# Kernel optimization log

Hardware: AMD Instinct MI355X
Metric: run time of the kernel (lower is better)

Reference implementation:

```python
import jax, jax.numpy as jnp
import numpy as np

MARGIN = 0.3
PD_EPS = 1e-6  # torch F.pairwise_distance adds eps to the difference


def setup_inputs() -> dict:
    key = jax.random.key(0)
    k1, k2 = jax.random.split(key)
    B, D, NUM_CLASSES = 8192, 256, 8
    embeddings = jax.random.normal(k1, (B, D), dtype=jnp.float32)
    labels = jax.random.randint(k2, (B,), 0, NUM_CLASSES, dtype=jnp.int64)
    return {"embeddings": embeddings, "labels": labels}


def _pairwise_euclidean(x):
    # cdist(x, x, p=2) via the Gram trick; clamp tiny negatives before sqrt
    sq = jnp.sum(x * x, axis=1)  # [B]
    d2 = sq[:, None] + sq[None, :] - 2.0 * (x @ x.T)
    return jnp.sqrt(jnp.maximum(d2, 0.0))


def reference(embeddings, labels):
    B = embeddings.shape[0]
    D = _pairwise_euclidean(embeddings)  # [B, B]

    eq = labels[:, None] == labels[None, :]
    eye = jnp.eye(B, dtype=bool)
    pos_mask = eq & ~eye          # same label, not self
    neg_mask = ~eq                # different label

    # hard mining: per anchor, farthest positive and closest negative
    pos_idx = jnp.argmax(jnp.where(pos_mask, D, -jnp.inf), axis=1)  # [B]
    neg_idx = jnp.argmin(jnp.where(neg_mask, D, jnp.inf), axis=1)   # [B]
    valid = pos_mask.any(axis=1) & neg_mask.any(axis=1)             # [B]

    # recompute triplet distances like F.pairwise_distance (eps on the diff)
    pos_dist = jnp.linalg.norm(embeddings - embeddings[pos_idx] + PD_EPS, axis=1)
    neg_dist = jnp.linalg.norm(embeddings - embeddings[neg_idx] + PD_EPS, axis=1)

    per_anchor = jax.nn.relu(pos_dist - neg_dist + MARGIN)
    n_valid = jnp.maximum(valid.sum(), 1)
    loss = jnp.sum(jnp.where(valid, per_anchor, 0.0)) / n_valid.astype(per_anchor.dtype)
    return loss
```

## Files before the change

kernel.cpp:

```cpp
#include <hip/hip_runtime.h>
#include <math.h>


typedef __attribute__((ext_vector_type(8))) short short8;
typedef __attribute__((ext_vector_type(4))) float floatx4;

#define B_N 8192
#define D_K 256

__device__ __forceinline__ unsigned short f2bf_rne(float f) {
  unsigned u = __float_as_uint(f);
  u += 0x7FFFu + ((u >> 16) & 1u);
  return (unsigned short)(u >> 16);
}

__global__ void k_split(const float* __restrict__ x, unsigned short* __restrict__ xhf,
                        float* __restrict__ sqq,
                        float* __restrict__ sum, int* __restrict__ cnt,
                        int* __restrict__ done) {
  __shared__ float sw[64];
  const int tid  = threadIdx.x;
  const int lane = tid & 63;
  const int w    = tid >> 6;
  const int b    = blockIdx.x;
  const int m    = lane & 15;
  const int quad = lane >> 4;
  const int row  = b * 16 + m;

  float s = 0.f;
#pragma unroll
  for (int h = 0; h < 2; ++h) {
    int tk = w + h * 4;
    int kk = tk * 32 + quad * 8;
    float4 f0 = *reinterpret_cast<const float4*>(x + (size_t)row * D_K + kk);
    float4 f1 = *reinterpret_cast<const float4*>(x + (size_t)row * D_K + kk + 4);
    s += f0.x * f0.x + f0.y * f0.y + f0.z * f0.z + f0.w * f0.w;
    s += f1.x * f1.x + f1.y * f1.y + f1.z * f1.z + f1.w * f1.w;
    ushort4 lo, hi;
    lo.x = f2bf_rne(f0.x); lo.y = f2bf_rne(f0.y); lo.z = f2bf_rne(f0.z); lo.w = f2bf_rne(f0.w);
    hi.x = f2bf_rne(f1.x); hi.y = f2bf_rne(f1.y); hi.z = f2bf_rne(f1.z); hi.w = f2bf_rne(f1.w);
    size_t o = ((size_t)b * 8 + tk) * 512 + lane * 8;
    *reinterpret_cast<ushort4*>(xhf + o)     = lo;
    *reinterpret_cast<ushort4*>(xhf + o + 4) = hi;
  }
  s += __shfl_xor(s, 16);
  s += __shfl_xor(s, 32);
  if (quad == 0) sw[w * 16 + m] = s;
  __syncthreads();
  if (tid < 16) {
    int i = b * 16 + tid;
    float t = sw[tid] + sw[16 + tid] + sw[32 + tid] + sw[48 + tid];
    sqq[i] = fmaf(t, 128.f, 262144.f);
  }
  if (b == 0 && tid == 0) { *sum = 0.f; *cnt = 0; *done = 0; }
}

__global__ __launch_bounds__(256) void k_mine15(
    const unsigned short* __restrict__ xhf, const int* __restrict__ lab,
    const float* __restrict__ sqq,
    unsigned* __restrict__ ppart, unsigned* __restrict__ npart) {
  __shared__ unsigned short Alds[8 * 8 * 512];

  int t  = blockIdx.x;
  int bi = (int)(64.5f - sqrtf(64.5f * 64.5f - 2.f * (float)t));
  int b0 = 64 * bi - (bi * (bi - 1)) / 2;
  if (t < b0) { bi--; b0 = 64 * bi - (bi * (bi - 1)) / 2; }
  else {
    int b1 = 64 * (bi + 1) - ((bi + 1) * bi) / 2;
    if (t >= b1) { bi++; b0 = b1; }
  }
  const int bj = bi + (t - b0);

  const int tid  = threadIdx.x;
  const int lane = tid & 63;
  const int w    = tid >> 6;
  const int wi   = w >> 1, wj = w & 1;
  const int quad = lane >> 4, l15 = lane & 15;
  const int i0   = bi * 128;

  {
    const short8* src = reinterpret_cast<const short8*>(xhf + (size_t)bi * 32768);
    short8* dst = reinterpret_cast<short8*>(Alds);
#pragma unroll
    for (int it = 0; it < 16; ++it) dst[it * 256 + tid] = src[it * 256 + tid];
  }

  unsigned pkey[16], nkey[16];
  unsigned lip0 = 0, lip1 = 0;
  float    sqi[16];
#pragma unroll
  for (int r = 0; r < 16; ++r) {
    pkey[r] = 0u; nkey[r] = 0xFFFFFFFFu;
    int ir = i0 + wi * 64 + (r >> 2) * 16 + quad * 4 + (r & 3);
    unsigned lv = (unsigned)lab[ir] & 0xFu;
    if (r < 8) lip0 |= lv << (r * 4); else lip1 |= lv << ((r - 8) * 4);
    sqi[r] = sqq[ir];
  }
  __syncthreads();

  const unsigned short* Bw = xhf + ((size_t)(bj * 8 + wj * 4) * 8) * 512 + lane * 8;
  const unsigned short* Aw = Alds + (size_t)wi * 32 * 512 + lane * 8;

  floatx4 acc[16];
#pragma unroll
  for (int q = 0; q < 16; ++q) acc[q] = (floatx4)0.f;

#pragma unroll
  for (int tk = 0; tk < 8; ++tk) {
    short8 Bf[4];
#pragma unroll
    for (int nt = 0; nt < 4; ++nt)
      Bf[nt] = *reinterpret_cast<const short8*>(Bw + nt * 4096 + tk * 512);
    short8 Af[4];
#pragma unroll
    for (int mt = 0; mt < 4; ++mt)
      Af[mt] = *reinterpret_cast<const short8*>(Aw + (size_t)(mt * 8 + tk) * 512);
#pragma unroll
    for (int mt = 0; mt < 4; ++mt)
#pragma unroll
      for (int nt = 0; nt < 4; ++nt)
        acc[mt * 4 + nt] = __builtin_amdgcn_mfma_f32_16x16x32_bf16(
            Af[mt], Bf[nt], acc[mt * 4 + nt], 0, 0, 0);
  }

#pragma unroll
  for (int nt = 0; nt < 4; ++nt) {
    int      j  = bj * 128 + wj * 64 + nt * 16 + l15;
    unsigned jl = (unsigned)lab[j] & 0xFu;
    float    sj = sqq[j];
    unsigned jp = 0u, jn = 0xFFFFFFFFu;
#pragma unroll
    for (int r = 0; r < 16; ++r) {
      int mt = r >> 2, reg = r & 3;
      float dot = acc[mt * 4 + nt][reg];
      int   ir  = i0 + wi * 64 + mt * 16 + quad * 4 + reg;
      unsigned lr = (r < 8 ? (lip0 >> (r * 4)) : (lip1 >> ((r - 8) * 4))) & 0xFu;
      bool eq = (jl == lr);
      unsigned kqi  = (unsigned)fmaf(-256.f, dot, sj);
      unsigned keyi = (kqi << 13) | (unsigned)j;
      unsigned pci = eq ? keyi : 0u;
      unsigned nci = eq ? 0xFFFFFFFFu : keyi;
      pkey[r] = pkey[r] > pci ? pkey[r] : pci;
      nkey[r] = nkey[r] < nci ? nkey[r] : nci;
      unsigned kqj  = (unsigned)fmaf(-256.f, dot, sqi[r]);
      unsigned keyj = (kqj << 13) | (unsigned)ir;
      unsigned pcj = eq ? keyj : 0u;
      unsigned ncj = eq ? 0xFFFFFFFFu : keyj;
      jp = jp > pcj ? jp : pcj;
      jn = jn < ncj ? jn : ncj;
    }
#pragma unroll
    for (int m = 16; m < 64; m <<= 1) {
      unsigned op = (unsigned)__shfl_xor((int)jp, m);
      unsigned on = (unsigned)__shfl_xor((int)jn, m);
      jp = jp > op ? jp : op;
      jn = jn < on ? jn : on;
    }
    if (quad == 0 && bi != bj) {
      size_t idx = (size_t)(2 * bi + wi) * B_N + j;
      ppart[idx] = jp;
      npart[idx] = jn;
    }
  }

#pragma unroll
  for (int r = 0; r < 16; ++r) {
    unsigned p = pkey[r], n = nkey[r];
#pragma unroll
    for (int m = 1; m < 16; m <<= 1) {
      unsigned op = (unsigned)__shfl_xor((int)p, m);
      unsigned on = (unsigned)__shfl_xor((int)n, m);
      p = p > op ? p : op;
      n = n < on ? n : on;
    }
    if (l15 == 0) {
      int ir = i0 + wi * 64 + (r >> 2) * 16 + quad * 4 + (r & 3);
      size_t idx = (size_t)(2 * bj + wj) * B_N + ir;
      ppart[idx] = p;
      npart[idx] = n;
    }
  }
}

__global__ void k_finish(const float* __restrict__ x,
                         const unsigned* __restrict__ ppart,
                         const unsigned* __restrict__ npart,
                         float* __restrict__ sum, int* __restrict__ cnt,
                         int* __restrict__ done, float* __restrict__ out) {
  __shared__ unsigned spk[32], snk[32];
  __shared__ float ssum[4];
  __shared__ int   scnt[4];
  const int tid = threadIdx.x;
  const int a0  = blockIdx.x * 32;

  if (tid < 32) { spk[tid] = 0u; snk[tid] = 0xFFFFFFFFu; }
  __syncthreads();

  {
    const int a    = a0 + (tid & 31);
    const int part = tid >> 5;
    unsigned p = 0u, n = 0xFFFFFFFFu;
#pragma unroll
    for (int s = 0; s < 16; ++s) {
      size_t idx = (size_t)(part * 16 + s) * B_N + a;
      unsigned pv = ppart[idx];
      unsigned nv = npart[idx];
      p = p > pv ? p : pv;
      n = n < nv ? n : nv;
    }
    atomicMax(&spk[tid & 31], p);
    atomicMin(&snk[tid & 31], n);
  }
  __syncthreads();

  const int w = tid >> 6, lane = tid & 63;
  float lsum = 0.f; int lcnt = 0;
#pragma unroll
  for (int it = 0; it < 8; ++it) {
    int al = w * 8 + it;
    int a  = a0 + al;
    unsigned p = spk[al];
    unsigned n = snk[al];
    bool valid = (p != 0u) && (n != 0xFFFFFFFFu);
    int  pidx = valid ? (int)(p & 8191u) : 0;
    int  nidx = valid ? (int)(n & 8191u) : 0;

    float4 xa = *reinterpret_cast<const float4*>(x + (size_t)a * D_K + lane * 4);
    float4 xp = *reinterpret_cast<const float4*>(x + (size_t)pidx * D_K + lane * 4);
    float4 xn = *reinterpret_cast<const float4*>(x + (size_t)nidx * D_K + lane * 4);
    float dx, sp = 0.f, sn = 0.f;
    dx = xa.x - xp.x + 1e-6f; sp = fmaf(dx, dx, sp);
    dx = xa.y - xp.y + 1e-6f; sp = fmaf(dx, dx, sp);
    dx = xa.z - xp.z + 1e-6f; sp = fmaf(dx, dx, sp);
    dx = xa.w - xp.w + 1e-6f; sp = fmaf(dx, dx, sp);
    dx = xa.x - xn.x + 1e-6f; sn = fmaf(dx, dx, sn);
    dx = xa.y - xn.y + 1e-6f; sn = fmaf(dx, dx, sn);
    dx = xa.z - xn.z + 1e-6f; sn = fmaf(dx, dx, sn);
    dx = xa.w - xn.w + 1e-6f; sn = fmaf(dx, dx, sn);
#pragma unroll
    for (int o = 32; o > 0; o >>= 1) {
      sp += __shfl_down(sp, o, 64);
      sn += __shfl_down(sn, o, 64);
    }
    if (lane == 0 && valid) {
      float per = sqrtf(sp) - sqrtf(sn) + 0.3f;
      if (per > 0.f) lsum += per;
      lcnt += 1;
    }
  }
  if (lane == 0) { ssum[w] = lsum; scnt[w] = lcnt; }
  __syncthreads();
  if (tid == 0) {
    atomicAdd(sum, ssum[0] + ssum[1] + ssum[2] + ssum[3]);
    atomicAdd(cnt, scnt[0] + scnt[1] + scnt[2] + scnt[3]);
    __threadfence();
    int prev = atomicAdd(done, 1);
    if (prev == gridDim.x - 1) {
      float s = atomicAdd(sum, 0.f);
      int   cc = atomicAdd(cnt, 0);
      if (cc < 1) cc = 1;
      out[0] = s / (float)cc;
    }
  }
}

extern "C" void kernel_launch(void* const* d_in, const int* in_sizes, int n_in,
                              void* d_out, int out_size, void* d_ws, size_t ws_size,
                              hipStream_t stream) {
  const float* x   = (const float*)d_in[0];
  const int*   lab = (const int*)d_in[1];
  float*       out = (float*)d_out;

  char* ws = (char*)d_ws;
  unsigned short* xhf = (unsigned short*)ws;
  float* sqq = (float*)(ws + (size_t)4608 * 1024);
  char*  pb = ws + (size_t)4608 * 1024 + 65536;
  size_t seg = (size_t)128 * B_N * 4;
  unsigned* ppart = (unsigned*)(pb);
  unsigned* npart = (unsigned*)(pb + seg);
  float* sum  = (float*)(pb + 2 * seg);
  int*   cnt  = (int*)(sum + 1);
  int*   done = (int*)(sum + 2);

  k_split<<<B_N / 16, 256, 0, stream>>>(x, xhf, sqq, sum, cnt, done);
  k_mine15<<<2080, 256, 0, stream>>>(xhf, lab, sqq, ppart, npart);
  k_finish<<<B_N / 32, 256, 0, stream>>>(x, ppart, npart, sum, cnt, done, out);
}
```

Baseline: 127.0 us.

## Split mining tile across 8 waves with LDS reduction of column partials

The mining kernel goes from 4 to 8 waves per 128x128 tile block, so each wave computes a 32x64 sub-tile instead of 64x64. This halves per-thread accumulator and key registers. Column-direction partial max/min results are combined across wave pairs through shared memory before being written out. The aim is more waves in flight to hide latency, at the cost of an extra barrier, more LDS use and the B fragment being loaded by twice as many waves.

Result: faster. 121.7 us (-4.1%).

```diff
diff --git a/kernel.cpp b/kernel.cpp
--- a/kernel.cpp
+++ b/kernel.cpp
@@ -55,11 +55,12 @@
   if (b == 0 && tid == 0) { *sum = 0.f; *cnt = 0; *done = 0; }
 }
 
-__global__ __launch_bounds__(256) void k_mine15(
+__global__ __launch_bounds__(512) void k_mine16(
     const unsigned short* __restrict__ xhf, const int* __restrict__ lab,
     const float* __restrict__ sqq,
     unsigned* __restrict__ ppart, unsigned* __restrict__ npart) {
   __shared__ unsigned short Alds[8 * 8 * 512];
+  __shared__ unsigned jbp[8 * 64], jbn[8 * 64];
 
   int t  = blockIdx.x;
   int bi = (int)(64.5f - sqrtf(64.5f * 64.5f - 2.f * (float)t));
@@ -74,7 +75,8 @@
   const int tid  = threadIdx.x;
   const int lane = tid & 63;
   const int w    = tid >> 6;
-  const int wi   = w >> 1, wj = w & 1;
+  const int wi   = w >> 1;
+  const int wj   = w & 1;
   const int quad = lane >> 4, l15 = lane & 15;
   const int i0   = bi * 128;
 
@@ -82,28 +84,27 @@
     const short8* src = reinterpret_cast<const short8*>(xhf + (size_t)bi * 32768);
     short8* dst = reinterpret_cast<short8*>(Alds);
 #pragma unroll
-    for (int it = 0; it < 16; ++it) dst[it * 256 + tid] = src[it * 256 + tid];
-  }
-
-  unsigned pkey[16], nkey[16];
-  unsigned lip0 = 0, lip1 = 0;
-  float    sqi[16];
-#pragma unroll
-  for (int r = 0; r < 16; ++r) {
+    for (int it = 0; it < 8; ++it) dst[it * 512 + tid] = src[it * 512 + tid];
+  }
+
+  unsigned pkey[8], nkey[8];
+  unsigned lip = 0;
+  float    sqi[8];
+#pragma unroll
+  for (int r = 0; r < 8; ++r) {
     pkey[r] = 0u; nkey[r] = 0xFFFFFFFFu;
-    int ir = i0 + wi * 64 + (r >> 2) * 16 + quad * 4 + (r & 3);
-    unsigned lv = (unsigned)lab[ir] & 0xFu;
-    if (r < 8) lip0 |= lv << (r * 4); else lip1 |= lv << ((r - 8) * 4);
+    int ir = i0 + wi * 32 + (r >> 2) * 16 + quad * 4 + (r & 3);
+    lip |= ((unsigned)lab[ir] & 0xFu) << (r * 4);
     sqi[r] = sqq[ir];
   }
   __syncthreads();
 
   const unsigned short* Bw = xhf + ((size_t)(bj * 8 + wj * 4) * 8) * 512 + lane * 8;
-  const unsigned short* Aw = Alds + (size_t)wi * 32 * 512 + lane * 8;
-
-  floatx4 acc[16];
-#pragma unroll
-  for (int q = 0; q < 16; ++q) acc[q] = (floatx4)0.f;
+  const unsigned short* Aw = Alds + (size_t)(wi * 2) * 8 * 512 + lane * 8;
+
+  floatx4 acc[8];
+#pragma unroll
+  for (int q = 0; q < 8; ++q) acc[q] = (floatx4)0.f;
 
 #pragma unroll
   for (int tk = 0; tk < 8; ++tk) {
@@ -111,12 +112,12 @@
 #pragma unroll
     for (int nt = 0; nt < 4; ++nt)
       Bf[nt] = *reinterpret_cast<const short8*>(Bw + nt * 4096 + tk * 512);
-    short8 Af[4];
-#pragma unroll
-    for (int mt = 0; mt < 4; ++mt)
+    short8 Af[2];
+#pragma unroll
+    for (int mt = 0; mt < 2; ++mt)
       Af[mt] = *reinterpret_cast<const short8*>(Aw + (size_t)(mt * 8 + tk) * 512);
 #pragma unroll
-    for (int mt = 0; mt < 4; ++mt)
+    for (int mt = 0; mt < 2; ++mt)
 #pragma unroll
       for (int nt = 0; nt < 4; ++nt)
         acc[mt * 4 + nt] = __builtin_amdgcn_mfma_f32_16x16x32_bf16(
@@ -130,12 +131,10 @@
     float    sj = sqq[j];
     unsigned jp = 0u, jn = 0xFFFFFFFFu;
 #pragma unroll
-    for (int r = 0; r < 16; ++r) {
-      int mt = r >> 2, reg = r & 3;
-      float dot = acc[mt * 4 + nt][reg];
-      int   ir  = i0 + wi * 64 + mt * 16 + quad * 4 + reg;
-      unsigned lr = (r < 8 ? (lip0 >> (r * 4)) : (lip1 >> ((r - 8) * 4))) & 0xFu;
-      bool eq = (jl == lr);
+    for (int r = 0; r < 8; ++r) {
+      float dot = acc[(r >> 2) * 4 + nt][r & 3];
+      int   ir  = i0 + wi * 32 + (r >> 2) * 16 + quad * 4 + (r & 3);
+      bool  eq  = (jl == ((lip >> (r * 4)) & 0xFu));
       unsigned kqi  = (unsigned)fmaf(-256.f, dot, sj);
       unsigned keyi = (kqi << 13) | (unsigned)j;
       unsigned pci = eq ? keyi : 0u;
@@ -156,15 +155,14 @@
       jp = jp > op ? jp : op;
       jn = jn < on ? jn : on;
     }
-    if (quad == 0 && bi != bj) {
-      size_t idx = (size_t)(2 * bi + wi) * B_N + j;
-      ppart[idx] = jp;
-      npart[idx] = jn;
-    }
-  }
-
-#pragma unroll
-  for (int r = 0; r < 16; ++r) {
+    if (quad == 0) {
+      jbp[w * 64 + nt * 16 + l15] = jp;
+      jbn[w * 64 + nt * 16 + l15] = jn;
+    }
+  }
+
+#pragma unroll
+  for (int r = 0; r < 8; ++r) {
     unsigned p = pkey[r], n = nkey[r];
 #pragma unroll
     for (int m = 1; m < 16; m <<= 1) {
@@ -174,11 +172,25 @@
       n = n < on ? n : on;
     }
     if (l15 == 0) {
-      int ir = i0 + wi * 64 + (r >> 2) * 16 + quad * 4 + (r & 3);
+      int ir = i0 + wi * 32 + (r >> 2) * 16 + quad * 4 + (r & 3);
       size_t idx = (size_t)(2 * bj + wj) * B_N + ir;
       ppart[idx] = p;
       npart[idx] = n;
     }
+  }
+
+  __syncthreads();
+  if ((wi & 1) == 0 && bi != bj) {
+    unsigned p = jbp[w * 64 + lane];
+    unsigned n = jbn[w * 64 + lane];
+    unsigned p2 = jbp[(w ^ 2) * 64 + lane];
+    unsigned n2 = jbn[(w ^ 2) * 64 + lane];
+    p = p > p2 ? p : p2;
+    n = n < n2 ? n : n2;
+    int j = bj * 128 + wj * 64 + lane;
+    size_t idx = (size_t)(2 * bi + (wi >> 1)) * B_N + j;
+    ppart[idx] = p;
+    npart[idx] = n;
   }
 }
 
@@ -283,6 +295,6 @@
   int*   done = (int*)(sum + 2);
 
   k_split<<<B_N / 16, 256, 0, stream>>>(x, xhf, sqq, sum, cnt, done);
-  k_mine15<<<2080, 256, 0, stream>>>(xhf, lab, sqq, ppart, npart);
+  k_mine16<<<2080, 512, 0, stream>>>(xhf, lab, sqq, ppart, npart);
   k_finish<<<B_N / 32, 256, 0, stream>>>(x, ppart, npart, sum, cnt, done, out);
 }
```

## Sort rows by label so each mining tile is pure positive or pure negative

Applied to the files above, without the earlier changes.

Adds a single-block counting-sort kernel that groups rows by label, padding each label group to a multiple of 128. The split and mining kernels then work in this permuted order. Each 128x128 tile is either same-label, tracking only the max, or different-label, tracking only the min. This halves the key state, comparisons and partial-result writes, and removes per-element label checks from the mining epilogue. In exchange it adds a serial single-block sort launch, extra padded tiles (72 instead of 64 blocks per side), and perm indirection in the finish kernel.

After: 153.6 us. +21.0%, slower.

```diff
diff --git a/kernel.cpp b/kernel.cpp
--- a/kernel.cpp
+++ b/kernel.cpp
@@ -5,8 +5,10 @@
 typedef __attribute__((ext_vector_type(8))) short short8;
 typedef __attribute__((ext_vector_type(4))) float floatx4;
 
-#define B_N 8192
-#define D_K 256
+#define B_N  8192
+#define BPAD 9216
+#define D_K  256
+#define NT   72
 
 __device__ __forceinline__ unsigned short f2bf_rne(float f) {
   unsigned u = __float_as_uint(f);
@@ -14,10 +16,77 @@
   return (unsigned short)(u >> 16);
 }
 
-__global__ void k_split(const float* __restrict__ x, unsigned short* __restrict__ xhf,
-                        float* __restrict__ sqq,
-                        float* __restrict__ sum, int* __restrict__ cnt,
-                        int* __restrict__ done) {
+__global__ void k_perm(const int* __restrict__ lab, int* __restrict__ perm,
+                       int* __restrict__ tb, int* __restrict__ Tdev,
+                       float* __restrict__ sum, int* __restrict__ cnt,
+                       int* __restrict__ done) {
+  __shared__ int lcnt[8][256];
+  __shared__ int c32[8][8];
+  __shared__ int S[8];
+  const int tid = threadIdx.x;
+
+  for (int i = tid; i < BPAD; i += 256) perm[i] = -1;
+
+  int ll[32], c[8];
+#pragma unroll
+  for (int l = 0; l < 8; ++l) c[l] = 0;
+  const int base = tid * 32;
+#pragma unroll
+  for (int k = 0; k < 32; ++k) { ll[k] = lab[base + k] & 7; c[ll[k]]++; }
+#pragma unroll
+  for (int l = 0; l < 8; ++l) lcnt[l][tid] = c[l];
+  __syncthreads();
+
+  if (tid < 64) {
+    int l = tid >> 3, g = tid & 7, s = 0;
+    for (int t2 = g * 32; t2 < g * 32 + 32; ++t2) s += lcnt[l][t2];
+    c32[l][g] = s;
+  }
+  __syncthreads();
+
+  if (tid == 0) {
+    int s = 0;
+    for (int l = 0; l < 8; ++l) {
+      int tot = 0;
+      for (int g = 0; g < 8; ++g) { int v = c32[l][g]; c32[l][g] = tot; tot += v; }
+      S[l] = s;
+      s += (tot + 127) & ~127;
+    }
+    int T = s >> 7;
+    Tdev[0] = T;
+    int l = 0, acc2 = 0, pl = 0;
+    for (int t = 0; t < T; ++t) {
+      while (t * 128 >= acc2 + ((l < 8) ? 0 : 0) && l < 8) {
+        int tot = (l + 1 < 8 ? S[l + 1] : s) - S[l];
+        if (t * 128 < S[l] + tot) break;
+        ++l;
+      }
+      tb[t] = l;
+      (void)acc2; (void)pl;
+    }
+    *sum = 0.f; *cnt = 0; *done = 0;
+  }
+  __syncthreads();
+
+  int ofs[8];
+  {
+    int g = tid >> 5;
+#pragma unroll
+    for (int l = 0; l < 8; ++l) ofs[l] = S[l] + c32[l][g];
+    for (int t2 = tid & ~31; t2 < tid; ++t2)
+#pragma unroll
+      for (int l = 0; l < 8; ++l) ofs[l] += lcnt[l][t2];
+  }
+#pragma unroll
+  for (int k = 0; k < 32; ++k) {
+    int l = ll[k];
+    perm[ofs[l]++] = base + k;
+  }
+}
+
+__global__ void k_split(const float* __restrict__ x, const int* __restrict__ perm,
+                        unsigned short* __restrict__ xhf,
+                        float* __restrict__ sqqP, float* __restrict__ sqqN) {
   __shared__ float sw[64];
   const int tid  = threadIdx.x;
   const int lane = tid & 63;
@@ -25,51 +94,61 @@
   const int b    = blockIdx.x;
   const int m    = lane & 15;
   const int quad = lane >> 4;
-  const int row  = b * 16 + m;
+  const int o    = perm[b * 16 + m];
 
   float s = 0.f;
 #pragma unroll
   for (int h = 0; h < 2; ++h) {
     int tk = w + h * 4;
     int kk = tk * 32 + quad * 8;
-    float4 f0 = *reinterpret_cast<const float4*>(x + (size_t)row * D_K + kk);
-    float4 f1 = *reinterpret_cast<const float4*>(x + (size_t)row * D_K + kk + 4);
+    float4 f0 = make_float4(0.f, 0.f, 0.f, 0.f), f1 = f0;
+    if (o >= 0) {
+      f0 = *reinterpret_cast<const float4*>(x + (size_t)o * D_K + kk);
+      f1 = *reinterpret_cast<const float4*>(x + (size_t)o * D_K + kk + 4);
+    }
     s += f0.x * f0.x + f0.y * f0.y + f0.z * f0.z + f0.w * f0.w;
     s += f1.x * f1.x + f1.y * f1.y + f1.z * f1.z + f1.w * f1.w;
     ushort4 lo, hi;
     lo.x = f2bf_rne(f0.x); lo.y = f2bf_rne(f0.y); lo.z = f2bf_rne(f0.z); lo.w = f2bf_rne(f0.w);
     hi.x = f2bf_rne(f1.x); hi.y = f2bf_rne(f1.y); hi.z = f2bf_rne(f1.z); hi.w = f2bf_rne(f1.w);
-    size_t o = ((size_t)b * 8 + tk) * 512 + lane * 8;
-    *reinterpret_cast<ushort4*>(xhf + o)     = lo;
-    *reinterpret_cast<ushort4*>(xhf + o + 4) = hi;
+    size_t oo = ((size_t)b * 8 + tk) * 512 + lane * 8;
+    *reinterpret_cast<ushort4*>(xhf + oo)     = lo;
+    *reinterpret_cast<ushort4*>(xhf + oo + 4) = hi;
   }
   s += __shfl_xor(s, 16);
   s += __shfl_xor(s, 32);
   if (quad == 0) sw[w * 16 + m] = s;
   __syncthreads();
   if (tid < 16) {
-    int i = b * 16 + tid;
+    int p  = b * 16 + tid;
+    int oo = perm[p];
     float t = sw[tid] + sw[16 + tid] + sw[32 + tid] + sw[48 + tid];
-    sqq[i] = fmaf(t, 128.f, 262144.f);
-  }
-  if (b == 0 && tid == 0) { *sum = 0.f; *cnt = 0; *done = 0; }
-}
-
-__global__ __launch_bounds__(256) void k_mine15(
-    const unsigned short* __restrict__ xhf, const int* __restrict__ lab,
-    const float* __restrict__ sqq,
-    unsigned* __restrict__ ppart, unsigned* __restrict__ npart) {
+    float q = fmaf(t, 64.f, 131072.f);
+    sqqP[p] = (oo >= 0) ? q : 0.f;
+    sqqN[p] = (oo >= 0) ? q : 262143.f;
+  }
+}
+
+__global__ __launch_bounds__(256) void k_mine17(
+    const unsigned short* __restrict__ xhf, const int* __restrict__ tb,
+    const int* __restrict__ Tdev,
+    const float* __restrict__ sqqP, const float* __restrict__ sqqN,
+    unsigned* __restrict__ part) {
   __shared__ unsigned short Alds[8 * 8 * 512];
 
   int t  = blockIdx.x;
-  int bi = (int)(64.5f - sqrtf(64.5f * 64.5f - 2.f * (float)t));
-  int b0 = 64 * bi - (bi * (bi - 1)) / 2;
-  if (t < b0) { bi--; b0 = 64 * bi - (bi * (bi - 1)) / 2; }
+  int bi = (int)(72.5f - sqrtf(72.5f * 72.5f - 2.f * (float)t));
+  int b0 = 72 * bi - (bi * (bi - 1)) / 2;
+  if (t < b0) { bi--; b0 = 72 * bi - (bi * (bi - 1)) / 2; }
   else {
-    int b1 = 64 * (bi + 1) - ((bi + 1) * bi) / 2;
+    int b1 = 72 * (bi + 1) - ((bi + 1) * bi) / 2;
     if (t >= b1) { bi++; b0 = b1; }
   }
   const int bj = bi + (t - b0);
+  const int T  = Tdev[0];
+  if (bj >= T) return;
+  const bool same = (tb[bi] == tb[bj]);
+  const float* __restrict__ sqc = same ? sqqP : sqqN;
 
   const int tid  = threadIdx.x;
   const int lane = tid & 63;
@@ -85,16 +164,13 @@
     for (int it = 0; it < 16; ++it) dst[it * 256 + tid] = src[it * 256 + tid];
   }
 
-  unsigned pkey[16], nkey[16];
-  unsigned lip0 = 0, lip1 = 0;
+  unsigned key[16];
   float    sqi[16];
 #pragma unroll
   for (int r = 0; r < 16; ++r) {
-    pkey[r] = 0u; nkey[r] = 0xFFFFFFFFu;
+    key[r] = same ? 0u : 0xFFFFFFFFu;
     int ir = i0 + wi * 64 + (r >> 2) * 16 + quad * 4 + (r & 3);
-    unsigned lv = (unsigned)lab[ir] & 0xFu;
-    if (r < 8) lip0 |= lv << (r * 4); else lip1 |= lv << ((r - 8) * 4);
-    sqi[r] = sqq[ir];
+    sqi[r] = sqc[ir];
   }
   __syncthreads();
 
@@ -123,90 +199,103 @@
             Af[mt], Bf[nt], acc[mt * 4 + nt], 0, 0, 0);
   }
 
-#pragma unroll
-  for (int nt = 0; nt < 4; ++nt) {
-    int      j  = bj * 128 + wj * 64 + nt * 16 + l15;
-    unsigned jl = (unsigned)lab[j] & 0xFu;
-    float    sj = sqq[j];
-    unsigned jp = 0u, jn = 0xFFFFFFFFu;
-#pragma unroll
-    for (int r = 0; r < 16; ++r) {
-      int mt = r >> 2, reg = r & 3;
-      float dot = acc[mt * 4 + nt][reg];
-      int   ir  = i0 + wi * 64 + mt * 16 + quad * 4 + reg;
-      unsigned lr = (r < 8 ? (lip0 >> (r * 4)) : (lip1 >> ((r - 8) * 4))) & 0xFu;
-      bool eq = (jl == lr);
-      unsigned kqi  = (unsigned)fmaf(-256.f, dot, sj);
-      unsigned keyi = (kqi << 13) | (unsigned)j;
-      unsigned pci = eq ? keyi : 0u;
-      unsigned nci = eq ? 0xFFFFFFFFu : keyi;
-      pkey[r] = pkey[r] > pci ? pkey[r] : pci;
-      nkey[r] = nkey[r] < nci ? nkey[r] : nci;
-      unsigned kqj  = (unsigned)fmaf(-256.f, dot, sqi[r]);
-      unsigned keyj = (kqj << 13) | (unsigned)ir;
-      unsigned pcj = eq ? keyj : 0u;
-      unsigned ncj = eq ? 0xFFFFFFFFu : keyj;
-      jp = jp > pcj ? jp : pcj;
-      jn = jn < ncj ? jn : ncj;
-    }
-#pragma unroll
-    for (int m = 16; m < 64; m <<= 1) {
-      unsigned op = (unsigned)__shfl_xor((int)jp, m);
-      unsigned on = (unsigned)__shfl_xor((int)jn, m);
-      jp = jp > op ? jp : op;
-      jn = jn < on ? jn : on;
-    }
-    if (quad == 0 && bi != bj) {
-      size_t idx = (size_t)(2 * bi + wi) * B_N + j;
-      ppart[idx] = jp;
-      npart[idx] = jn;
+  if (same) {
+#pragma unroll
+    for (int nt = 0; nt < 4; ++nt) {
+      int   j  = bj * 128 + wj * 64 + nt * 16 + l15;
+      float sj = sqc[j];
+      unsigned jp = 0u;
+#pragma unroll
+      for (int r = 0; r < 16; ++r) {
+        float dot = acc[(r >> 2) * 4 + nt][r & 3];
+        int   ir  = i0 + wi * 64 + (r >> 2) * 16 + quad * 4 + (r & 3);
+        unsigned keyi = ((unsigned)fmaf(-128.f, dot, sj) << 14) | (unsigned)j;
+        key[r] = key[r] > keyi ? key[r] : keyi;
+        unsigned keyj = ((unsigned)fmaf(-128.f, dot, sqi[r]) << 14) | (unsigned)ir;
+        jp = jp > keyj ? jp : keyj;
+      }
+#pragma unroll
+      for (int m = 16; m < 64; m <<= 1) {
+        unsigned op = (unsigned)__shfl_xor((int)jp, m);
+        jp = jp > op ? jp : op;
+      }
+      if (quad == 0 && bi != bj)
+        part[(size_t)(2 * bi + wi) * BPAD + j] = jp;
+    }
+  } else {
+#pragma unroll
+    for (int nt = 0; nt < 4; ++nt) {
+      int   j  = bj * 128 + wj * 64 + nt * 16 + l15;
+      float sj = sqc[j];
+      unsigned jn = 0xFFFFFFFFu;
+#pragma unroll
+      for (int r = 0; r < 16; ++r) {
+        float dot = acc[(r >> 2) * 4 + nt][r & 3];
+        int   ir  = i0 + wi * 64 + (r >> 2) * 16 + quad * 4 + (r & 3);
+        unsigned keyi = ((unsigned)fmaf(-128.f, dot, sj) << 14) | (unsigned)j;
+        key[r] = key[r] < keyi ? key[r] : keyi;
+        unsigned keyj = ((unsigned)fmaf(-128.f, dot, sqi[r]) << 14) | (unsigned)ir;
+        jn = jn < keyj ? jn : keyj;
+      }
+#pragma unroll
+      for (int m = 16; m < 64; m <<= 1) {
+        unsigned on = (unsigned)__shfl_xor((int)jn, m);
+        jn = jn < on ? jn : on;
+      }
+      if (quad == 0)
+        part[(size_t)(2 * bi + wi) * BPAD + j] = jn;
     }
   }
 
 #pragma unroll
   for (int r = 0; r < 16; ++r) {
-    unsigned p = pkey[r], n = nkey[r];
-#pragma unroll
-    for (int m = 1; m < 16; m <<= 1) {
-      unsigned op = (unsigned)__shfl_xor((int)p, m);
-      unsigned on = (unsigned)__shfl_xor((int)n, m);
-      p = p > op ? p : op;
-      n = n < on ? n : on;
+    unsigned p = key[r];
+    if (same) {
+#pragma unroll
+      for (int m = 1; m < 16; m <<= 1) {
+        unsigned op = (unsigned)__shfl_xor((int)p, m);
+        p = p > op ? p : op;
+      }
+    } else {
+#pragma unroll
+      for (int m = 1; m < 16; m <<= 1) {
+        unsigned op = (unsigned)__shfl_xor((int)p, m);
+        p = p < op ? p : op;
+      }
     }
     if (l15 == 0) {
       int ir = i0 + wi * 64 + (r >> 2) * 16 + quad * 4 + (r & 3);
-      size_t idx = (size_t)(2 * bj + wj) * B_N + ir;
-      ppart[idx] = p;
-      npart[idx] = n;
-    }
-  }
-}
-
-__global__ void k_finish(const float* __restrict__ x,
-                         const unsigned* __restrict__ ppart,
-                         const unsigned* __restrict__ npart,
+      part[(size_t)(2 * bj + wj) * BPAD + ir] = p;
+    }
+  }
+}
+
+__global__ void k_finish(const float* __restrict__ x, const int* __restrict__ perm,
+                         const int* __restrict__ tb, const int* __restrict__ Tdev,
+                         const unsigned* __restrict__ part,
                          float* __restrict__ sum, int* __restrict__ cnt,
                          int* __restrict__ done, float* __restrict__ out) {
   __shared__ unsigned spk[32], snk[32];
   __shared__ float ssum[4];
   __shared__ int   scnt[4];
-  const int tid = threadIdx.x;
-  const int a0  = blockIdx.x * 32;
+  const int tid  = threadIdx.x;
+  const int a0   = blockIdx.x * 32;
+  const int T    = Tdev[0];
+  const int myb  = tb[a0 >> 7];
 
   if (tid < 32) { spk[tid] = 0u; snk[tid] = 0xFFFFFFFFu; }
   __syncthreads();
 
   {
     const int a    = a0 + (tid & 31);
-    const int part = tid >> 5;
+    const int g    = tid >> 5;
     unsigned p = 0u, n = 0xFFFFFFFFu;
-#pragma unroll
-    for (int s = 0; s < 16; ++s) {
-      size_t idx = (size_t)(part * 16 + s) * B_N + a;
-      unsigned pv = ppart[idx];
-      unsigned nv = npart[idx];
-      p = p > pv ? p : pv;
-      n = n < nv ? n : nv;
+    int send = g * 18 + 18;
+    if (send > 2 * T) send = 2 * T;
+    for (int s = g * 18; s < send; ++s) {
+      unsigned v = part[(size_t)s * BPAD + a];
+      if (tb[s >> 1] == myb) { p = p > v ? p : v; }
+      else                   { n = n < v ? n : v; }
     }
     atomicMax(&spk[tid & 31], p);
     atomicMin(&snk[tid & 31], n);
@@ -214,18 +303,20 @@
   __syncthreads();
 
   const int w = tid >> 6, lane = tid & 63;
-  float lsum = 0.f; int lcnt = 0;
+  float lsum = 0.f; int lcnt2 = 0;
 #pragma unroll
   for (int it = 0; it < 8; ++it) {
     int al = w * 8 + it;
     int a  = a0 + al;
+    int o  = perm[a];
     unsigned p = spk[al];
     unsigned n = snk[al];
-    bool valid = (p != 0u) && (n != 0xFFFFFFFFu);
-    int  pidx = valid ? (int)(p & 8191u) : 0;
-    int  nidx = valid ? (int)(n & 8191u) : 0;
-
-    float4 xa = *reinterpret_cast<const float4*>(x + (size_t)a * D_K + lane * 4);
+    bool valid = (o >= 0) && (p != 0u) && (n != 0xFFFFFFFFu);
+    int  pidx = valid ? perm[p & 16383u] : 0;
+    int  nidx = valid ? perm[n & 16383u] : 0;
+    int  ao   = valid ? o : 0;
+
+    float4 xa = *reinterpret_cast<const float4*>(x + (size_t)ao * D_K + lane * 4);
     float4 xp = *reinterpret_cast<const float4*>(x + (size_t)pidx * D_K + lane * 4);
     float4 xn = *reinterpret_cast<const float4*>(x + (size_t)nidx * D_K + lane * 4);
     float dx, sp = 0.f, sn = 0.f;
@@ -238,17 +329,17 @@
     dx = xa.z - xn.z + 1e-6f; sn = fmaf(dx, dx, sn);
     dx = xa.w - xn.w + 1e-6f; sn = fmaf(dx, dx, sn);
 #pragma unroll
-    for (int o = 32; o > 0; o >>= 1) {
-      sp += __shfl_down(sp, o, 64);
-      sn += __shfl_down(sn, o, 64);
+    for (int o2 = 32; o2 > 0; o2 >>= 1) {
+      sp += __shfl_down(sp, o2, 64);
+      sn += __shfl_down(sn, o2, 64);
     }
     if (lane == 0 && valid) {
       float per = sqrtf(sp) - sqrtf(sn) + 0.3f;
       if (per > 0.f) lsum += per;
-      lcnt += 1;
-    }
-  }
-  if (lane == 0) { ssum[w] = lsum; scnt[w] = lcnt; }
+      lcnt2 += 1;
+    }
+  }
+  if (lane == 0) { ssum[w] = lsum; scnt[w] = lcnt2; }
   __syncthreads();
   if (tid == 0) {
     atomicAdd(sum, ssum[0] + ssum[1] + ssum[2] + ssum[3]);
@@ -273,16 +364,18 @@
 
   char* ws = (char*)d_ws;
   unsigned short* xhf = (unsigned short*)ws;
-  float* sqq = (float*)(ws + (size_t)4608 * 1024);
-  char*  pb = ws + (size_t)4608 * 1024 + 65536;
-  size_t seg = (size_t)128 * B_N * 4;
-  unsigned* ppart = (unsigned*)(pb);
-  unsigned* npart = (unsigned*)(pb + seg);
-  float* sum  = (float*)(pb + 2 * seg);
+  float* sqqP = (float*)(ws + (size_t)4608 * 1024);
+  float* sqqN = (float*)(ws + (size_t)4648 * 1024);
+  int*   perm = (int*)(ws + (size_t)4688 * 1024);
+  int*   tb   = (int*)(ws + (size_t)4728 * 1024);
+  int*   Tdev = (int*)(ws + (size_t)4729 * 1024);
+  unsigned* part = (unsigned*)(ws + (size_t)4732 * 1024);
+  float* sum  = (float*)(ws + (size_t)9920 * 1024);
   int*   cnt  = (int*)(sum + 1);
   int*   done = (int*)(sum + 2);
 
-  k_split<<<B_N / 16, 256, 0, stream>>>(x, xhf, sqq, sum, cnt, done);
-  k_mine15<<<2080, 256, 0, stream>>>(xhf, lab, sqq, ppart, npart);
-  k_finish<<<B_N / 32, 256, 0, stream>>>(x, ppart, npart, sum, cnt, done, out);
-}
+  k_perm<<<1, 256, 0, stream>>>(lab, perm, tb, Tdev, sum, cnt, done);
+  k_split<<<BPAD / 16, 256, 0, stream>>>(x, perm, xhf, sqqP, sqqN);
+  k_mine17<<<NT * (NT + 1) / 2, 256, 0, stream>>>(xhf, tb, Tdev, sqqP, sqqN, part);
+  k_finish<<<BPAD / 32, 256, 0, stream>>>(x, perm, tb, Tdev, part, sum, cnt, done, out);
+}
```
